# Optimization experiments

Hardware: AMD Instinct MI355X
Metric: run time of the kernel (lower is better)

## Reference

```python
import jax, jax.numpy as jnp
import numpy as np

NUM_HEADS = 12
STEP_SIZE = 3

def softmax_1(a):
    # exp(a_i) / (1 + sum_j exp(a_j)), numerically stable
    m = jnp.maximum(jnp.max(a, axis=-1, keepdims=True), 0.0)
    e = jnp.exp(a - m)
    return e / (jnp.exp(-m) + jnp.sum(e, axis=-1, keepdims=True))

def setup_inputs() -> dict:
    key = jax.random.key(0)
    ks = jax.random.split(key, 7)
    B, N, C, L = 16, 4096, 768, 16
    s = C ** -0.5
    return {
        "x": jax.random.normal(ks[0], (B, N, C), dtype=jnp.float32),
        "query": jax.random.normal(ks[1], (1, L, C), dtype=jnp.float32),
        "Wq": jax.random.normal(ks[2], (C, C), dtype=jnp.float32) * s,
        "Wk": jax.random.normal(ks[3], (C, C), dtype=jnp.float32) * s,
        "Wv": jax.random.normal(ks[4], (C, C), dtype=jnp.float32) * s,
        "Wproj": jax.random.normal(ks[5], (C, C), dtype=jnp.float32) * s,
        "b_proj": jnp.zeros((C,), dtype=jnp.float32),
    }

def reference(x, query, Wq, Wk, Wv, Wproj, b_proj):
    B, N, C = x.shape
    H = NUM_HEADS
    hd = C // H
    L = query.shape[1]
    scale = hd ** -0.5
    # learned queries broadcast over batch
    queries = jnp.broadcast_to(query, (B, L, C))
    q = (queries @ Wq.T).reshape(B, L, H, hd).transpose(0, 2, 1, 3)  # [B,H,L,hd]
    k = (x @ Wk.T).reshape(B, N, H, hd).transpose(0, 2, 1, 3)        # [B,H,N,hd]
    v = k  # Hopfield update: state retrieves against stored patterns k
    for _ in range(STEP_SIZE):
        qs = q * scale
        attn = jnp.einsum('bhld,bhnd->bhln', qs, k)  # [B,H,L,N]
        attn = softmax_1(attn)
        q = jnp.einsum('bhln,bhnd->bhld', attn, v)   # [B,H,L,hd]
    out = q.transpose(0, 2, 1, 3).reshape(B, L, C)
    out = out @ Wv.T          # self.v output projection (no bias)
    out = out @ Wproj.T + b_proj  # self.proj
    return out
```

## Files before the change

kernel.cpp:

```cpp
#include <hip/hip_runtime.h>


typedef float  float4v  __attribute__((ext_vector_type(4)));
typedef short  short4v  __attribute__((ext_vector_type(4)));
typedef short  short8v  __attribute__((ext_vector_type(8)));
typedef unsigned int uint4v __attribute__((ext_vector_type(4)));
typedef short8v bf16x8;

__device__ __forceinline__ void splitbf(float v, unsigned int& hi, unsigned int& lo){
  unsigned int u = __float_as_uint(v);
  hi = u >> 16;
  float r = v - __uint_as_float(u & 0xffff0000u);
  lo = (__float_as_uint(r) + 0x8000u) >> 16;
}
__device__ __forceinline__ unsigned int packbf(float v){
  unsigned int u = __float_as_uint(v);
  float r = v - __uint_as_float(u & 0xffff0000u);
  return (u >> 16) | ((__float_as_uint(r) + 0x8000u) & 0xffff0000u);
}

__global__ __launch_bounds__(256)
void cvt_planar_kernel(const float* __restrict__ src, unsigned short* __restrict__ dh,
                       unsigned short* __restrict__ dl){
  size_t idx = (size_t)blockIdx.x*256 + threadIdx.x;
  float4v v = ((const float4v*)src)[idx];
  short4v h4, l4;
  #pragma unroll
  for(int e=0;e<4;e++){
    unsigned int hh, ll;
    splitbf(v[e], hh, ll);
    h4[e] = (short)hh;
    l4[e] = (short)ll;
  }
  ((short4v*)dh)[idx] = h4;
  ((short4v*)dl)[idx] = l4;
}

__global__ __launch_bounds__(256)
void q0_kernel(const float* __restrict__ query, const float* __restrict__ wq,
               float* __restrict__ q0){
  int idx = blockIdx.x*256 + threadIdx.x;
  int l = idx / 768, c = idx - l*768;
  const float* qr = query + l*768;
  const float* wr = wq + (size_t)c*768;
  float s = 0.f;
  for(int j=0;j<768;j+=4){
    float4v a  = *(const float4v*)(qr+j);
    float4v w4 = *(const float4v*)(wr+j);
    s += a[0]*w4[0]+a[1]*w4[1]+a[2]*w4[2]+a[3]*w4[3];
  }
  q0[idx] = s;
}

__global__ __launch_bounds__(256, 3)
void gemm_k_kernel(const float* __restrict__ x, const unsigned short* __restrict__ wh,
                   const unsigned short* __restrict__ wl, unsigned int* __restrict__ khead){
  __shared__ unsigned short Ah[512*8], Al[512*8];
  const int tid  = threadIdx.x;
  const int id   = blockIdx.x;
  const int xcd  = id & 7, slot = id >> 3;
  const int bml  = slot / 6;
  const int bn   = slot - bml*6;
  const int bm   = xcd*64 + bml;
  const int wave = tid >> 6, lane = tid & 63, quad = lane >> 4, l16 = lane & 15;

  float4v acc[8][2];
  #pragma unroll
  for(int i=0;i<8;i++)
    #pragma unroll
    for(int j=0;j<2;j++) acc[i][j] = (float4v){0.f,0.f,0.f,0.f};

  const float* xA = x + (size_t)bm*128*768;
  const unsigned short* wbh = wh + (size_t)(bn*128 + wave*32 + l16)*768 + quad*8;
  const unsigned short* wbl = wl + (size_t)(bn*128 + wave*32 + l16)*768 + quad*8;

  const int row0 = tid >> 2, c8 = tid & 3;
  const int C0 = row0*4 + (c8 ^ ((row0 >> 2) & 3));
  const int C1 = C0 + 256;
  const float* g0 = xA + (size_t)row0*768 + c8*8;
  const float* g1 = g0 + (size_t)64*768;
  const int crd = l16*4 + (quad ^ ((l16 >> 2) & 3));

  float4v p00 = *(const float4v*)(g0);
  float4v p01 = *(const float4v*)(g0 + 4);
  float4v p10 = *(const float4v*)(g1);
  float4v p11 = *(const float4v*)(g1 + 4);

  for(int k0=0;k0<768;k0+=32){
    bf16x8 b_h[2], b_l[2];
    #pragma unroll
    for(int j=0;j<2;j++){
      b_h[j] = *(const bf16x8*)(wbh + (size_t)j*16*768 + k0);
      b_l[j] = *(const bf16x8*)(wbl + (size_t)j*16*768 + k0);
    }
    __syncthreads();

    {
      short8v hv, lv;
      #pragma unroll
      for(int e=0;e<4;e++){
        unsigned int hh, ll;
        splitbf(p00[e], hh, ll); hv[e]   = (short)hh; lv[e]   = (short)ll;
        splitbf(p01[e], hh, ll); hv[e+4] = (short)hh; lv[e+4] = (short)ll;
      }
      *(short8v*)(Ah + C0*8) = hv;
      *(short8v*)(Al + C0*8) = lv;
      #pragma unroll
      for(int e=0;e<4;e++){
        unsigned int hh, ll;
        splitbf(p10[e], hh, ll); hv[e]   = (short)hh; lv[e]   = (short)ll;
        splitbf(p11[e], hh, ll); hv[e+4] = (short)hh; lv[e+4] = (short)ll;
      }
      *(short8v*)(Ah + C1*8) = hv;
      *(short8v*)(Al + C1*8) = lv;
    }
    __syncthreads();

    if(k0 + 32 < 768){
      p00 = *(const float4v*)(g0 + k0 + 32);
      p01 = *(const float4v*)(g0 + k0 + 36);
      p10 = *(const float4v*)(g1 + k0 + 32);
      p11 = *(const float4v*)(g1 + k0 + 36);
    }

    #pragma unroll
    for(int i=0;i<8;i++){
      const unsigned short* ap = Ah + (size_t)(i*64 + crd)*8;
      const unsigned short* lp = Al + (size_t)(i*64 + crd)*8;
      bf16x8 a_h = *(const bf16x8*)ap;
      bf16x8 a_l = *(const bf16x8*)lp;
      #pragma unroll
      for(int j=0;j<2;j++){
        acc[i][j] = __builtin_amdgcn_mfma_f32_16x16x32_bf16(a_h, b_h[j], acc[i][j],0,0,0);
        acc[i][j] = __builtin_amdgcn_mfma_f32_16x16x32_bf16(a_l, b_h[j], acc[i][j],0,0,0);
        acc[i][j] = __builtin_amdgcn_mfma_f32_16x16x32_bf16(a_h, b_l[j], acc[i][j],0,0,0);
      }
    }
  }
  const int b     = bm >> 5;
  const int Cbase = bn*128 + wave*32;
  const int h     = Cbase >> 6;
  const int dbase = Cbase & 63;
  const int nn0   = (bm & 31)*128;
  unsigned int* kout = khead + ((size_t)(b*12 + h)*4096 + nn0)*64 + dbase;
  #pragma unroll
  for(int i=0;i<8;i++)
    #pragma unroll
    for(int j=0;j<2;j++)
      #pragma unroll
      for(int r=0;r<4;r++)
        kout[(size_t)(i*16 + quad*4 + r)*64 + j*16 + l16] = packbf(acc[i][j][r]);
}

__global__ __launch_bounds__(512, 2)
void attn3_kernel(const unsigned int* __restrict__ khead,
                  const float* __restrict__ q0g, float* __restrict__ qcur){
  __shared__ unsigned int knd[256*64];
  float* accf  = (float*)knd;
  float* lredf = (float*)knd + 8192;
  float* qtmp  = (float*)knd + 8320;

  const int tid  = threadIdx.x;
  const int bh   = blockIdx.x;
  const int b    = bh / 12;
  const int h    = bh - b*12;
  const int wave = tid >> 6, lane = tid & 63, quad = lane >> 4, l16 = lane & 15;

  const unsigned int* kb = khead + (size_t)(b*12 + h)*4096*64;
  const int srow = tid >> 1, scol = (tid & 1)*32;
  const int sphi = ((srow & 7) << 2) ^ ((srow & 8) << 1);
  const unsigned int* kbt = kb + (size_t)srow*64 + scol;

  const int rowA = wave*32 + ((l16 >> 2) << 3) + (l16 & 3);
  const int rowB = rowA + 4;
  const int phiA = ((l16 & 3) << 2) ^ (((l16 >> 2) & 1) << 4);
  const int phiB = phiA ^ 16;
  const int q1   = quad & 1;

  uint4v pf[8];
  #pragma unroll
  for(int g=0; g<8; ++g) pf[g] = *(const uint4v*)(kbt + g*4);

  for(int iter = 0; iter < 3; ++iter){
    const float* qrow = (iter == 0) ? (q0g + (size_t)l16*768 + h*64)
                                    : (qtmp + l16*64);
    bf16x8 qh[2], ql[2];
    #pragma unroll
    for(int s = 0; s < 2; ++s){
      float4v v0 = *(const float4v*)(qrow + s*32 + quad*8);
      float4v v1 = *(const float4v*)(qrow + s*32 + quad*8 + 4);
      #pragma unroll
      for(int e = 0; e < 8; ++e){
        float v = (e < 4 ? v0[e] : v1[e-4]) * 0.125f;
        unsigned int hh, ll;
        splitbf(v, hh, ll);
        qh[s][e] = (short)hh;
        ql[s][e] = (short)ll;
      }
    }
    __syncthreads();

    float4v acc[4];
    #pragma unroll
    for(int j=0;j<4;j++) acc[j] = (float4v){0.f,0.f,0.f,0.f};
    float lsum = 0.f;

    for(int t = 0; t < 16; ++t){
      #pragma unroll
      for(int g=0; g<8; ++g)
        *(uint4v*)(knd + srow*64 + ((scol + g*4) ^ sphi)) = pf[g];
      if(!(iter == 2 && t == 15)){
        const int tn = (t + 1) & 15;
        #pragma unroll
        for(int g=0; g<8; ++g) pf[g] = *(const uint4v*)(kbt + (size_t)tn*16384 + g*4);
      }

      float4v s1 = (float4v){0.f,0.f,0.f,0.f};
      float4v s2 = (float4v){0.f,0.f,0.f,0.f};
      #pragma unroll
      for(int s = 0; s < 2; ++s){
        const int c0 = s*32 + quad*8;
        uint4v w0 = *(const uint4v*)(knd + rowA*64 + ((c0    ) ^ phiA));
        uint4v w1 = *(const uint4v*)(knd + rowA*64 + ((c0 + 4) ^ phiA));
        uint4v u0 = *(const uint4v*)(knd + rowB*64 + ((c0    ) ^ phiB));
        uint4v u1 = *(const uint4v*)(knd + rowB*64 + ((c0 + 4) ^ phiB));
        bf16x8 a1h, a1l, a2h, a2l;
        #pragma unroll
        for(int j = 0; j < 4; ++j){
          a1h[j]   = (short)(w0[j] & 0xffffu);  a1l[j]   = (short)(w0[j] >> 16);
          a1h[j+4] = (short)(w1[j] & 0xffffu);  a1l[j+4] = (short)(w1[j] >> 16);
          a2h[j]   = (short)(u0[j] & 0xffffu);  a2l[j]   = (short)(u0[j] >> 16);
          a2h[j+4] = (short)(u1[j] & 0xffffu);  a2l[j+4] = (short)(u1[j] >> 16);
        }
        s1 = __builtin_amdgcn_mfma_f32_16x16x32_bf16(a1h, qh[s], s1, 0,0,0);
        s1 = __builtin_amdgcn_mfma_f32_16x16x32_bf16(a1l, qh[s], s1, 0,0,0);
        s1 = __builtin_amdgcn_mfma_f32_16x16x32_bf16(a1h, ql[s], s1, 0,0,0);
        s2 = __builtin_amdgcn_mfma_f32_16x16x32_bf16(a2h, qh[s], s2, 0,0,0);
        s2 = __builtin_amdgcn_mfma_f32_16x16x32_bf16(a2l, qh[s], s2, 0,0,0);
        s2 = __builtin_amdgcn_mfma_f32_16x16x32_bf16(a2h, ql[s], s2, 0,0,0);
      }

      bf16x8 pa_h, pa_l;
      #pragma unroll
      for(int e = 0; e < 4; ++e){
        float v = __expf(s1[e]);
        lsum += v;
        unsigned int hh, ll;
        splitbf(v, hh, ll);
        pa_h[e] = (short)hh;
        pa_l[e] = (short)ll;
        float v2 = __expf(s2[e]);
        lsum += v2;
        splitbf(v2, hh, ll);
        pa_h[e+4] = (short)hh;
        pa_l[e+4] = (short)ll;
      }

      const int rb0 = wave*32 + quad*8;
      #pragma unroll
      for(int j = 0; j < 4; ++j){
        bf16x8 kbh, kbl;
        #pragma unroll
        for(int e = 0; e < 8; ++e){
          const int jx = ((e >> 2) ^ q1) & 1;
          unsigned int w = knd[(rb0 + e)*64 + ((j ^ jx) << 4) + (l16 ^ ((e & 3) << 2))];
          kbh[e] = (short)(w & 0xffffu);
          kbl[e] = (short)(w >> 16);
        }
        acc[j] = __builtin_amdgcn_mfma_f32_16x16x32_bf16(pa_h, kbh, acc[j], 0,0,0);
        acc[j] = __builtin_amdgcn_mfma_f32_16x16x32_bf16(pa_l, kbh, acc[j], 0,0,0);
        acc[j] = __builtin_amdgcn_mfma_f32_16x16x32_bf16(pa_h, kbl, acc[j], 0,0,0);
      }
    }

    __syncthreads();
    lsum += __shfl_xor(lsum, 16);
    lsum += __shfl_xor(lsum, 32);
    if(quad == 0) lredf[wave*16 + l16] = lsum;
    #pragma unroll
    for(int j = 0; j < 4; ++j)
      #pragma unroll
      for(int r = 0; r < 4; ++r)
        accf[wave*1024 + (quad*4 + r)*64 + j*16 + l16] = acc[j][r];
    __syncthreads();
    #pragma unroll
    for(int k = 0; k < 2; ++k){
      const int i = tid + k*512;
      const int l = i >> 6, d = i & 63;
      float s = 0.f, lt = 1.f;
      #pragma unroll
      for(int w = 0; w < 8; ++w){ s += accf[w*1024 + i]; }
      #pragma unroll
      for(int w = 0; w < 8; ++w){ lt += lredf[w*16 + l]; }
      const float qv = s / lt;
      if(iter < 2) qtmp[i] = qv;
      else qcur[(size_t)(b*16 + l)*768 + h*64 + d] = qv;
    }
    __syncthreads();
  }
}

__global__ __launch_bounds__(256)
void proj_kernel(const float* __restrict__ inp, const float* __restrict__ w,
                 const float* __restrict__ bias, float* __restrict__ out){
  __shared__ float rows[4*768];
  const int r0 = blockIdx.x*4;
  const int c  = blockIdx.y*256 + threadIdx.x;
  for(int j = threadIdx.x; j < 4*768; j += 256) rows[j] = inp[(size_t)r0*768 + j];
  __syncthreads();
  const float* wr = w + (size_t)c*768;
  float a0=0.f, a1=0.f, a2=0.f, a3=0.f;
  for(int j=0;j<768;j+=4){
    float4v w4 = *(const float4v*)(wr+j);
    float4v r0v = *(const float4v*)(rows+j);
    float4v r1v = *(const float4v*)(rows+768+j);
    float4v r2v = *(const float4v*)(rows+1536+j);
    float4v r3v = *(const float4v*)(rows+2304+j);
    #pragma unroll
    for(int e=0;e<4;e++){
      a0 += r0v[e]*w4[e]; a1 += r1v[e]*w4[e];
      a2 += r2v[e]*w4[e]; a3 += r3v[e]*w4[e];
    }
  }
  const float bb = bias ? bias[c] : 0.f;
  out[(size_t)(r0+0)*768 + c] = a0 + bb;
  out[(size_t)(r0+1)*768 + c] = a1 + bb;
  out[(size_t)(r0+2)*768 + c] = a2 + bb;
  out[(size_t)(r0+3)*768 + c] = a3 + bb;
}

extern "C" void kernel_launch(void* const* d_in, const int* in_sizes, int n_in,
                              void* d_out, int out_size, void* d_ws, size_t ws_size,
                              hipStream_t stream){
  const float* x     = (const float*)d_in[0];
  const float* query = (const float*)d_in[1];
  const float* Wq    = (const float*)d_in[2];
  const float* Wk    = (const float*)d_in[3];
  const float* Wv    = (const float*)d_in[4];
  const float* Wproj = (const float*)d_in[5];
  const float* bproj = (const float*)d_in[6];
  float* out = (float*)d_out;

  char* ws = (char*)d_ws;
  unsigned int*   khead = (unsigned int*)(ws);
  float*          qcur  = (float*)(ws + 201326592);
  float*          q0    = (float*)(ws + 202113024);
  char*           R     = ws + 202162176;
  unsigned short* wkh   = (unsigned short*)(R);
  unsigned short* wkl   = (unsigned short*)(R + 1179648);
  float*          out1  = (float*)(R);

  cvt_planar_kernel<<<576, 256, 0, stream>>>(Wk, wkh, wkl);
  q0_kernel<<<48, 256, 0, stream>>>(query, Wq, q0);
  gemm_k_kernel<<<3072, 256, 0, stream>>>(x, wkh, wkl, khead);

  attn3_kernel<<<192, 512, 0, stream>>>(khead, q0, qcur);

  proj_kernel<<<dim3(64, 3), 256, 0, stream>>>(qcur, Wv, nullptr, out1);
  proj_kernel<<<dim3(64, 3), 256, 0, stream>>>(out1, Wproj, bproj, out);
}
```

Baseline: 682.6 us.

## Double-buffer LDS tiles in K-projection GEMM with one barrier per step

The K-projection GEMM now ping-pongs between two LDS buffers. Each step converts and stores the next x tile into one buffer while running MFMAs on the other, so there is one barrier per k-step instead of two. Global loads for x and the weight fragments are issued two and one steps ahead. This raises LDS use to 32KB per block and adds register pressure, which could lower occupancy under the 3-blocks-per-CU launch bound.

Result: slower. 784.8 us (+15.0%).

```diff
diff --git a/kernel.cpp b/kernel.cpp
--- a/kernel.cpp
+++ b/kernel.cpp
@@ -52,10 +52,52 @@
   q0[idx] = s;
 }
 
+__device__ __forceinline__ void conv_store(unsigned short* __restrict__ AhW,
+                                           unsigned short* __restrict__ AlW,
+                                           int C0, int C1,
+                                           float4v p0, float4v p1, float4v p2, float4v p3){
+  short8v hv, lv;
+  #pragma unroll
+  for(int e=0;e<4;e++){
+    unsigned int hh, ll;
+    splitbf(p0[e], hh, ll); hv[e]   = (short)hh; lv[e]   = (short)ll;
+    splitbf(p1[e], hh, ll); hv[e+4] = (short)hh; lv[e+4] = (short)ll;
+  }
+  *(short8v*)(AhW + C0*8) = hv;
+  *(short8v*)(AlW + C0*8) = lv;
+  #pragma unroll
+  for(int e=0;e<4;e++){
+    unsigned int hh, ll;
+    splitbf(p2[e], hh, ll); hv[e]   = (short)hh; lv[e]   = (short)ll;
+    splitbf(p3[e], hh, ll); hv[e+4] = (short)hh; lv[e+4] = (short)ll;
+  }
+  *(short8v*)(AhW + C1*8) = hv;
+  *(short8v*)(AlW + C1*8) = lv;
+}
+
+__device__ __forceinline__ void mfma_phase(const unsigned short* __restrict__ AhR,
+                                           const unsigned short* __restrict__ AlR,
+                                           int crd,
+                                           bf16x8 bh0, bf16x8 bh1, bf16x8 bl0, bf16x8 bl1,
+                                           float4v (&acc)[8][2]){
+  #pragma unroll
+  for(int i=0;i<8;i++){
+    bf16x8 a_h = *(const bf16x8*)(AhR + (size_t)(i*64 + crd)*8);
+    bf16x8 a_l = *(const bf16x8*)(AlR + (size_t)(i*64 + crd)*8);
+    acc[i][0] = __builtin_amdgcn_mfma_f32_16x16x32_bf16(a_h, bh0, acc[i][0],0,0,0);
+    acc[i][0] = __builtin_amdgcn_mfma_f32_16x16x32_bf16(a_l, bh0, acc[i][0],0,0,0);
+    acc[i][0] = __builtin_amdgcn_mfma_f32_16x16x32_bf16(a_h, bl0, acc[i][0],0,0,0);
+    acc[i][1] = __builtin_amdgcn_mfma_f32_16x16x32_bf16(a_h, bh1, acc[i][1],0,0,0);
+    acc[i][1] = __builtin_amdgcn_mfma_f32_16x16x32_bf16(a_l, bh1, acc[i][1],0,0,0);
+    acc[i][1] = __builtin_amdgcn_mfma_f32_16x16x32_bf16(a_h, bl1, acc[i][1],0,0,0);
+  }
+}
+
 __global__ __launch_bounds__(256, 3)
 void gemm_k_kernel(const float* __restrict__ x, const unsigned short* __restrict__ wh,
                    const unsigned short* __restrict__ wl, unsigned int* __restrict__ khead){
-  __shared__ unsigned short Ah[512*8], Al[512*8];
+  __shared__ unsigned short Ah0[512*8], Al0[512*8];
+  __shared__ unsigned short Ah1[512*8], Al1[512*8];
   const int tid  = threadIdx.x;
   const int id   = blockIdx.x;
   const int xcd  = id & 7, slot = id >> 3;
@@ -81,62 +123,42 @@
   const float* g1 = g0 + (size_t)64*768;
   const int crd = l16*4 + (quad ^ ((l16 >> 2) & 3));
 
-  float4v p00 = *(const float4v*)(g0);
-  float4v p01 = *(const float4v*)(g0 + 4);
-  float4v p10 = *(const float4v*)(g1);
-  float4v p11 = *(const float4v*)(g1 + 4);
-
-  for(int k0=0;k0<768;k0+=32){
-    bf16x8 b_h[2], b_l[2];
-    #pragma unroll
-    for(int j=0;j<2;j++){
-      b_h[j] = *(const bf16x8*)(wbh + (size_t)j*16*768 + k0);
-      b_l[j] = *(const bf16x8*)(wbl + (size_t)j*16*768 + k0);
-    }
-    __syncthreads();
-
+  float4v pA0, pA1, pA2, pA3, pB0, pB1, pB2, pB3;
+  bf16x8 bCh0, bCh1, bCl0, bCl1, bNh0, bNh1, bNl0, bNl1;
+  pA0 = *(const float4v*)(g0);      pA1 = *(const float4v*)(g0 + 4);
+  pA2 = *(const float4v*)(g1);      pA3 = *(const float4v*)(g1 + 4);
+  pB0 = *(const float4v*)(g0 + 32); pB1 = *(const float4v*)(g0 + 36);
+  pB2 = *(const float4v*)(g1 + 32); pB3 = *(const float4v*)(g1 + 36);
+  bCh0 = *(const bf16x8*)(wbh);          bCh1 = *(const bf16x8*)(wbh + 12288);
+  bCl0 = *(const bf16x8*)(wbl);          bCl1 = *(const bf16x8*)(wbl + 12288);
+  conv_store(Ah0, Al0, C0, C1, pA0, pA1, pA2, pA3);
+  __syncthreads();
+
+  for(int i = 0; i < 12; ++i){
     {
-      short8v hv, lv;
-      #pragma unroll
-      for(int e=0;e<4;e++){
-        unsigned int hh, ll;
-        splitbf(p00[e], hh, ll); hv[e]   = (short)hh; lv[e]   = (short)ll;
-        splitbf(p01[e], hh, ll); hv[e+4] = (short)hh; lv[e+4] = (short)ll;
-      }
-      *(short8v*)(Ah + C0*8) = hv;
-      *(short8v*)(Al + C0*8) = lv;
-      #pragma unroll
-      for(int e=0;e<4;e++){
-        unsigned int hh, ll;
-        splitbf(p10[e], hh, ll); hv[e]   = (short)hh; lv[e]   = (short)ll;
-        splitbf(p11[e], hh, ll); hv[e+4] = (short)hh; lv[e+4] = (short)ll;
-      }
-      *(short8v*)(Ah + C1*8) = hv;
-      *(short8v*)(Al + C1*8) = lv;
-    }
-    __syncthreads();
-
-    if(k0 + 32 < 768){
-      p00 = *(const float4v*)(g0 + k0 + 32);
-      p01 = *(const float4v*)(g0 + k0 + 36);
-      p10 = *(const float4v*)(g1 + k0 + 32);
-      p11 = *(const float4v*)(g1 + k0 + 36);
-    }
-
-    #pragma unroll
-    for(int i=0;i<8;i++){
-      const unsigned short* ap = Ah + (size_t)(i*64 + crd)*8;
-      const unsigned short* lp = Al + (size_t)(i*64 + crd)*8;
-      bf16x8 a_h = *(const bf16x8*)ap;
-      bf16x8 a_l = *(const bf16x8*)lp;
-      #pragma unroll
-      for(int j=0;j<2;j++){
-        acc[i][j] = __builtin_amdgcn_mfma_f32_16x16x32_bf16(a_h, b_h[j], acc[i][j],0,0,0);
-        acc[i][j] = __builtin_amdgcn_mfma_f32_16x16x32_bf16(a_l, b_h[j], acc[i][j],0,0,0);
-        acc[i][j] = __builtin_amdgcn_mfma_f32_16x16x32_bf16(a_h, b_l[j], acc[i][j],0,0,0);
-      }
-    }
-  }
+      const int ka = (2*i + 2 < 24) ? (2*i + 2)*32 : 736;
+      const int kb = (2*i + 1)*32;
+      pA0 = *(const float4v*)(g0 + ka); pA1 = *(const float4v*)(g0 + ka + 4);
+      pA2 = *(const float4v*)(g1 + ka); pA3 = *(const float4v*)(g1 + ka + 4);
+      bNh0 = *(const bf16x8*)(wbh + kb); bNh1 = *(const bf16x8*)(wbh + 12288 + kb);
+      bNl0 = *(const bf16x8*)(wbl + kb); bNl1 = *(const bf16x8*)(wbl + 12288 + kb);
+      conv_store(Ah1, Al1, C0, C1, pB0, pB1, pB2, pB3);
+      mfma_phase(Ah0, Al0, crd, bCh0, bCh1, bCl0, bCl1, acc);
+      __syncthreads();
+    }
+    {
+      const int ka = (2*i + 3 < 24) ? (2*i + 3)*32 : 736;
+      const int kb = (2*i + 2 < 24) ? (2*i + 2)*32 : 736;
+      pB0 = *(const float4v*)(g0 + ka); pB1 = *(const float4v*)(g0 + ka + 4);
+      pB2 = *(const float4v*)(g1 + ka); pB3 = *(const float4v*)(g1 + ka + 4);
+      bCh0 = *(const bf16x8*)(wbh + kb); bCh1 = *(const bf16x8*)(wbh + 12288 + kb);
+      bCl0 = *(const bf16x8*)(wbl + kb); bCl1 = *(const bf16x8*)(wbl + 12288 + kb);
+      conv_store(Ah0, Al0, C0, C1, pA0, pA1, pA2, pA3);
+      mfma_phase(Ah1, Al1, crd, bNh0, bNh1, bNl0, bNl1, acc);
+      __syncthreads();
+    }
+  }
+
   const int b     = bm >> 5;
   const int Cbase = bn*128 + wave*32;
   const int h     = Cbase >> 6;
```

## Split Hopfield attention over N into four chunks with atomic cross-block reduction

Applied to the files above, without the earlier changes.

The single attention kernel that ran all three Hopfield iterations in one block per (batch, head) is split into a per-iteration partial kernel. It launches four blocks per (batch, head), each covering a quarter of the keys, and accumulates partial outputs and softmax denominators with global atomics. A small reduce kernel then normalizes and resets the accumulators. This raises the grid from 192 to 768 blocks to fill the GPU's compute units. The cost is extra kernel launches, atomic traffic and nondeterministic float summation order.

After: 810.1 us. 18.7% more time.

```diff
diff --git a/kernel.cpp b/kernel.cpp
--- a/kernel.cpp
+++ b/kernel.cpp
@@ -52,6 +52,11 @@
   q0[idx] = s;
 }
 
+__global__ __launch_bounds__(512)
+void zero_kernel(float* __restrict__ p){
+  p[(size_t)blockIdx.x*512 + threadIdx.x] = 0.f;
+}
+
 __global__ __launch_bounds__(256, 3)
 void gemm_k_kernel(const float* __restrict__ x, const unsigned short* __restrict__ wh,
                    const unsigned short* __restrict__ wl, unsigned int* __restrict__ khead){
@@ -152,21 +157,23 @@
         kout[(size_t)(i*16 + quad*4 + r)*64 + j*16 + l16] = packbf(acc[i][j][r]);
 }
 
-__global__ __launch_bounds__(512, 2)
-void attn3_kernel(const unsigned int* __restrict__ khead,
-                  const float* __restrict__ q0g, float* __restrict__ qcur){
+__global__ __launch_bounds__(512, 4)
+void attn_part_kernel(const unsigned int* __restrict__ khead,
+                      const float* __restrict__ q0g,
+                      const float* __restrict__ qred,
+                      int first,
+                      float* __restrict__ gacc, float* __restrict__ glsum){
   __shared__ unsigned int knd[256*64];
   float* accf  = (float*)knd;
   float* lredf = (float*)knd + 8192;
-  float* qtmp  = (float*)knd + 8320;
-
-  const int tid  = threadIdx.x;
-  const int bh   = blockIdx.x;
-  const int b    = bh / 12;
-  const int h    = bh - b*12;
-  const int wave = tid >> 6, lane = tid & 63, quad = lane >> 4, l16 = lane & 15;
-
-  const unsigned int* kb = khead + (size_t)(b*12 + h)*4096*64;
+
+  const int tid   = threadIdx.x;
+  const int bh    = blockIdx.x >> 2;
+  const int chunk = blockIdx.x & 3;
+  const int h     = bh - (bh/12)*12;
+  const int wave  = tid >> 6, lane = tid & 63, quad = lane >> 4, l16 = lane & 15;
+
+  const unsigned int* kb = khead + (size_t)bh*4096*64 + (size_t)chunk*4*16384;
   const int srow = tid >> 1, scol = (tid & 1)*32;
   const int sphi = ((srow & 7) << 2) ^ ((srow & 8) << 1);
   const unsigned int* kbt = kb + (size_t)srow*64 + scol;
@@ -177,127 +184,143 @@
   const int phiB = phiA ^ 16;
   const int q1   = quad & 1;
 
+  const float* qrow = first ? (q0g + (size_t)l16*768 + h*64)
+                            : (qred + (size_t)bh*1024 + l16*64);
+  bf16x8 qh[2], ql[2];
+  #pragma unroll
+  for(int s = 0; s < 2; ++s){
+    float4v v0 = *(const float4v*)(qrow + s*32 + quad*8);
+    float4v v1 = *(const float4v*)(qrow + s*32 + quad*8 + 4);
+    #pragma unroll
+    for(int e = 0; e < 8; ++e){
+      float v = (e < 4 ? v0[e] : v1[e-4]) * 0.125f;
+      unsigned int hh, ll;
+      splitbf(v, hh, ll);
+      qh[s][e] = (short)hh;
+      ql[s][e] = (short)ll;
+    }
+  }
+
   uint4v pf[8];
   #pragma unroll
   for(int g=0; g<8; ++g) pf[g] = *(const uint4v*)(kbt + g*4);
 
-  for(int iter = 0; iter < 3; ++iter){
-    const float* qrow = (iter == 0) ? (q0g + (size_t)l16*768 + h*64)
-                                    : (qtmp + l16*64);
-    bf16x8 qh[2], ql[2];
+  float4v acc[4];
+  #pragma unroll
+  for(int j=0;j<4;j++) acc[j] = (float4v){0.f,0.f,0.f,0.f};
+  float lsum = 0.f;
+
+  for(int t = 0; t < 4; ++t){
+    #pragma unroll
+    for(int g=0; g<8; ++g)
+      *(uint4v*)(knd + srow*64 + ((scol + g*4) ^ sphi)) = pf[g];
+    if(t < 3){
+      #pragma unroll
+      for(int g=0; g<8; ++g) pf[g] = *(const uint4v*)(kbt + (size_t)(t+1)*16384 + g*4);
+    }
+
+    float4v s1 = (float4v){0.f,0.f,0.f,0.f};
+    float4v s2 = (float4v){0.f,0.f,0.f,0.f};
     #pragma unroll
     for(int s = 0; s < 2; ++s){
-      float4v v0 = *(const float4v*)(qrow + s*32 + quad*8);
-      float4v v1 = *(const float4v*)(qrow + s*32 + quad*8 + 4);
+      const int c0 = s*32 + quad*8;
+      uint4v w0 = *(const uint4v*)(knd + rowA*64 + ((c0    ) ^ phiA));
+      uint4v w1 = *(const uint4v*)(knd + rowA*64 + ((c0 + 4) ^ phiA));
+      uint4v u0 = *(const uint4v*)(knd + rowB*64 + ((c0    ) ^ phiB));
+      uint4v u1 = *(const uint4v*)(knd + rowB*64 + ((c0 + 4) ^ phiB));
+      bf16x8 a1h, a1l, a2h, a2l;
+      #pragma unroll
+      for(int j = 0; j < 4; ++j){
+        a1h[j]   = (short)(w0[j] & 0xffffu);  a1l[j]   = (short)(w0[j] >> 16);
+        a1h[j+4] = (short)(w1[j] & 0xffffu);  a1l[j+4] = (short)(w1[j] >> 16);
+        a2h[j]   = (short)(u0[j] & 0xffffu);  a2l[j]   = (short)(u0[j] >> 16);
+        a2h[j+4] = (short)(u1[j] & 0xffffu);  a2l[j+4] = (short)(u1[j] >> 16);
+      }
+      s1 = __builtin_amdgcn_mfma_f32_16x16x32_bf16(a1h, qh[s], s1, 0,0,0);
+      s1 = __builtin_amdgcn_mfma_f32_16x16x32_bf16(a1l, qh[s], s1, 0,0,0);
+      s1 = __builtin_amdgcn_mfma_f32_16x16x32_bf16(a1h, ql[s], s1, 0,0,0);
+      s2 = __builtin_amdgcn_mfma_f32_16x16x32_bf16(a2h, qh[s], s2, 0,0,0);
+      s2 = __builtin_amdgcn_mfma_f32_16x16x32_bf16(a2l, qh[s], s2, 0,0,0);
+      s2 = __builtin_amdgcn_mfma_f32_16x16x32_bf16(a2h, ql[s], s2, 0,0,0);
+    }
+
+    bf16x8 pa_h, pa_l;
+    #pragma unroll
+    for(int e = 0; e < 4; ++e){
+      float v = __expf(s1[e]);
+      lsum += v;
+      unsigned int hh, ll;
+      splitbf(v, hh, ll);
+      pa_h[e] = (short)hh;
+      pa_l[e] = (short)ll;
+      float v2 = __expf(s2[e]);
+      lsum += v2;
+      splitbf(v2, hh, ll);
+      pa_h[e+4] = (short)hh;
+      pa_l[e+4] = (short)ll;
+    }
+
+    const int rb0 = wave*32 + quad*8;
+    #pragma unroll
+    for(int j = 0; j < 4; ++j){
+      bf16x8 kbh, kbl;
       #pragma unroll
       for(int e = 0; e < 8; ++e){
-        float v = (e < 4 ? v0[e] : v1[e-4]) * 0.125f;
-        unsigned int hh, ll;
-        splitbf(v, hh, ll);
-        qh[s][e] = (short)hh;
-        ql[s][e] = (short)ll;
-      }
-    }
-    __syncthreads();
-
-    float4v acc[4];
-    #pragma unroll
-    for(int j=0;j<4;j++) acc[j] = (float4v){0.f,0.f,0.f,0.f};
-    float lsum = 0.f;
-
-    for(int t = 0; t < 16; ++t){
-      #pragma unroll
-      for(int g=0; g<8; ++g)
-        *(uint4v*)(knd + srow*64 + ((scol + g*4) ^ sphi)) = pf[g];
-      if(!(iter == 2 && t == 15)){
-        const int tn = (t + 1) & 15;
-        #pragma unroll
-        for(int g=0; g<8; ++g) pf[g] = *(const uint4v*)(kbt + (size_t)tn*16384 + g*4);
-      }
-
-      float4v s1 = (float4v){0.f,0.f,0.f,0.f};
-      float4v s2 = (float4v){0.f,0.f,0.f,0.f};
-      #pragma unroll
-      for(int s = 0; s < 2; ++s){
-        const int c0 = s*32 + quad*8;
-        uint4v w0 = *(const uint4v*)(knd + rowA*64 + ((c0    ) ^ phiA));
-        uint4v w1 = *(const uint4v*)(knd + rowA*64 + ((c0 + 4) ^ phiA));
-        uint4v u0 = *(const uint4v*)(knd + rowB*64 + ((c0    ) ^ phiB));
-        uint4v u1 = *(const uint4v*)(knd + rowB*64 + ((c0 + 4) ^ phiB));
-        bf16x8 a1h, a1l, a2h, a2l;
-        #pragma unroll
-        for(int j = 0; j < 4; ++j){
-          a1h[j]   = (short)(w0[j] & 0xffffu);  a1l[j]   = (short)(w0[j] >> 16);
-          a1h[j+4] = (short)(w1[j] & 0xffffu);  a1l[j+4] = (short)(w1[j] >> 16);
-          a2h[j]   = (short)(u0[j] & 0xffffu);  a2l[j]   = (short)(u0[j] >> 16);
-          a2h[j+4] = (short)(u1[j] & 0xffffu);  a2l[j+4] = (short)(u1[j] >> 16);
-        }
-        s1 = __builtin_amdgcn_mfma_f32_16x16x32_bf16(a1h, qh[s], s1, 0,0,0);
-        s1 = __builtin_amdgcn_mfma_f32_16x16x32_bf16(a1l, qh[s], s1, 0,0,0);
-        s1 = __builtin_amdgcn_mfma_f32_16x16x32_bf16(a1h, ql[s], s1, 0,0,0);
-        s2 = __builtin_amdgcn_mfma_f32_16x16x32_bf16(a2h, qh[s], s2, 0,0,0);
-        s2 = __builtin_amdgcn_mfma_f32_16x16x32_bf16(a2l, qh[s], s2, 0,0,0);
-        s2 = __builtin_amdgcn_mfma_f32_16x16x32_bf16(a2h, ql[s], s2, 0,0,0);
-      }
-
-      bf16x8 pa_h, pa_l;
-      #pragma unroll
-      for(int e = 0; e < 4; ++e){
-        float v = __expf(s1[e]);
-        lsum += v;
-        unsigned int hh, ll;
-        splitbf(v, hh, ll);
-        pa_h[e] = (short)hh;
-        pa_l[e] = (short)ll;
-        float v2 = __expf(s2[e]);
-        lsum += v2;
-        splitbf(v2, hh, ll);
-        pa_h[e+4] = (short)hh;
-        pa_l[e+4] = (short)ll;
-      }
-
-      const int rb0 = wave*32 + quad*8;
-      #pragma unroll
-      for(int j = 0; j < 4; ++j){
-        bf16x8 kbh, kbl;
-        #pragma unroll
-        for(int e = 0; e < 8; ++e){
-          const int jx = ((e >> 2) ^ q1) & 1;
-          unsigned int w = knd[(rb0 + e)*64 + ((j ^ jx) << 4) + (l16 ^ ((e & 3) << 2))];
-          kbh[e] = (short)(w & 0xffffu);
-          kbl[e] = (short)(w >> 16);
-        }
-        acc[j] = __builtin_amdgcn_mfma_f32_16x16x32_bf16(pa_h, kbh, acc[j], 0,0,0);
-        acc[j] = __builtin_amdgcn_mfma_f32_16x16x32_bf16(pa_l, kbh, acc[j], 0,0,0);
-        acc[j] = __builtin_amdgcn_mfma_f32_16x16x32_bf16(pa_h, kbl, acc[j], 0,0,0);
-      }
-    }
-
-    __syncthreads();
-    lsum += __shfl_xor(lsum, 16);
-    lsum += __shfl_xor(lsum, 32);
-    if(quad == 0) lredf[wave*16 + l16] = lsum;
-    #pragma unroll
-    for(int j = 0; j < 4; ++j)
-      #pragma unroll
-      for(int r = 0; r < 4; ++r)
-        accf[wave*1024 + (quad*4 + r)*64 + j*16 + l16] = acc[j][r];
-    __syncthreads();
-    #pragma unroll
-    for(int k = 0; k < 2; ++k){
-      const int i = tid + k*512;
-      const int l = i >> 6, d = i & 63;
-      float s = 0.f, lt = 1.f;
-      #pragma unroll
-      for(int w = 0; w < 8; ++w){ s += accf[w*1024 + i]; }
-      #pragma unroll
-      for(int w = 0; w < 8; ++w){ lt += lredf[w*16 + l]; }
-      const float qv = s / lt;
-      if(iter < 2) qtmp[i] = qv;
-      else qcur[(size_t)(b*16 + l)*768 + h*64 + d] = qv;
-    }
-    __syncthreads();
-  }
+        const int jx = ((e >> 2) ^ q1) & 1;
+        unsigned int w = knd[(rb0 + e)*64 + ((j ^ jx) << 4) + (l16 ^ ((e & 3) << 2))];
+        kbh[e] = (short)(w & 0xffffu);
+        kbl[e] = (short)(w >> 16);
+      }
+      acc[j] = __builtin_amdgcn_mfma_f32_16x16x32_bf16(pa_h, kbh, acc[j], 0,0,0);
+      acc[j] = __builtin_amdgcn_mfma_f32_16x16x32_bf16(pa_l, kbh, acc[j], 0,0,0);
+      acc[j] = __builtin_amdgcn_mfma_f32_16x16x32_bf16(pa_h, kbl, acc[j], 0,0,0);
+    }
+  }
+
+  __syncthreads();
+  lsum += __shfl_xor(lsum, 16);
+  lsum += __shfl_xor(lsum, 32);
+  if(quad == 0) lredf[wave*16 + l16] = lsum;
+  #pragma unroll
+  for(int j = 0; j < 4; ++j)
+    #pragma unroll
+    for(int r = 0; r < 4; ++r)
+      accf[wave*1024 + (quad*4 + r)*64 + j*16 + l16] = acc[j][r];
+  __syncthreads();
+  #pragma unroll
+  for(int k = 0; k < 2; ++k){
+    const int i = tid + k*512;
+    float s = 0.f;
+    #pragma unroll
+    for(int w = 0; w < 8; ++w){ s += accf[w*1024 + i]; }
+    atomicAdd(&gacc[(size_t)bh*1024 + i], s);
+  }
+  if(tid < 16){
+    float lt = 0.f;
+    #pragma unroll
+    for(int w = 0; w < 8; ++w){ lt += lredf[w*16 + tid]; }
+    atomicAdd(&glsum[bh*16 + tid], lt);
+  }
+}
+
+__global__ __launch_bounds__(256)
+void attn_reduce_kernel(float* __restrict__ gacc, float* __restrict__ glsum,
+                        float* __restrict__ qred, float* __restrict__ qcur,
+                        int final){
+  const int bh = blockIdx.x;
+  const int b  = bh / 12, h = bh - b*12;
+  #pragma unroll
+  for(int k = 0; k < 4; ++k){
+    const int i = threadIdx.x + k*256;
+    const int l = i >> 6, d = i & 63;
+    const float s  = gacc[(size_t)bh*1024 + i];
+    const float lt = 1.f + glsum[bh*16 + l];
+    const float qv = s / lt;
+    if(final) qcur[(size_t)(b*16 + l)*768 + h*64 + d] = qv;
+    else      qred[(size_t)bh*1024 + i] = qv;
+    gacc[(size_t)bh*1024 + i] = 0.f;
+  }
+  if(threadIdx.x < 16) glsum[bh*16 + threadIdx.x] = 0.f;
 }
 
 __global__ __launch_bounds__(256)
@@ -348,13 +371,23 @@
   char*           R     = ws + 202162176;
   unsigned short* wkh   = (unsigned short*)(R);
   unsigned short* wkl   = (unsigned short*)(R + 1179648);
+  float*          gacc  = (float*)(R);
+  float*          glsum = (float*)(R + 786432);
+  float*          qred  = (float*)(R + 798720);
   float*          out1  = (float*)(R);
 
   cvt_planar_kernel<<<576, 256, 0, stream>>>(Wk, wkh, wkl);
   q0_kernel<<<48, 256, 0, stream>>>(query, Wq, q0);
   gemm_k_kernel<<<3072, 256, 0, stream>>>(x, wkh, wkl, khead);
 
-  attn3_kernel<<<192, 512, 0, stream>>>(khead, q0, qcur);
+  zero_kernel<<<390, 512, 0, stream>>>(gacc);
+
+  for(int it = 0; it < 3; ++it){
+    attn_part_kernel<<<768, 512, 0, stream>>>(khead, q0, qred, it == 0 ? 1 : 0,
+                                              gacc, glsum);
+    attn_reduce_kernel<<<192, 256, 0, stream>>>(gacc, glsum, qred, qcur,
+                                                it == 2 ? 1 : 0);
+  }
 
   proj_kernel<<<dim3(64, 3), 256, 0, stream>>>(qcur, Wv, nullptr, out1);
   proj_kernel<<<dim3(64, 3), 256, 0, stream>>>(out1, Wproj, bproj, out);
```

## Load K tiles straight into double-buffered LDS with pre-swizzled layout

Applied to the files above, without the earlier changes.

The K-projection kernel now writes K in an LDS-ready tiled layout, with the XOR swizzle already applied per 256-row tile. The attention kernel then uses global_load_lds to DMA each tile directly into one of two LDS buffers, waiting only on vmcnt. This removes the register staging of prefetched K and the separate LDS store pass, and overlaps the next tile's load with compute on the current one. In exchange, the K buffer doubles to 128KB of LDS, which likely cuts the two-blocks-per-CU occupancy requested by the launch bounds down to one. It also relies on each wave reading only the rows it loaded itself, since there is no block barrier between tiles.

Result: faster. 663.6 us (-2.8%).

```diff
diff --git a/kernel.cpp b/kernel.cpp
--- a/kernel.cpp
+++ b/kernel.cpp
@@ -17,6 +17,12 @@
   unsigned int u = __float_as_uint(v);
   float r = v - __uint_as_float(u & 0xffff0000u);
   return (u >> 16) | ((__float_as_uint(r) + 0x8000u) & 0xffff0000u);
+}
+
+__device__ __forceinline__ void gll16(const unsigned int* g, unsigned int* l){
+  __builtin_amdgcn_global_load_lds(
+      (const __attribute__((address_space(1))) unsigned int*)g,
+      (__attribute__((address_space(3))) unsigned int*)l, 16, 0, 0);
 }
 
 __global__ __launch_bounds__(256)
@@ -142,23 +148,29 @@
   const int h     = Cbase >> 6;
   const int dbase = Cbase & 63;
   const int nn0   = (bm & 31)*128;
-  unsigned int* kout = khead + ((size_t)(b*12 + h)*4096 + nn0)*64 + dbase;
+  unsigned int* kout = khead + (size_t)(b*12 + h)*262144;
   #pragma unroll
-  for(int i=0;i<8;i++)
-    #pragma unroll
-    for(int j=0;j<2;j++)
-      #pragma unroll
-      for(int r=0;r<4;r++)
-        kout[(size_t)(i*16 + quad*4 + r)*64 + j*16 + l16] = packbf(acc[i][j][r]);
+  for(int i=0;i<8;i++){
+    #pragma unroll
+    for(int r=0;r<4;r++){
+      const int n   = nn0 + i*16 + quad*4 + r;
+      const int row = n & 255, t = n >> 8;
+      const int ph  = ((row & 7) << 2) ^ ((row & 8) << 1);
+      unsigned int* kr = kout + (size_t)t*16384 + row*64;
+      #pragma unroll
+      for(int j=0;j<2;j++)
+        kr[(dbase + j*16 + l16) ^ ph] = packbf(acc[i][j][r]);
+    }
+  }
 }
 
 __global__ __launch_bounds__(512, 2)
 void attn3_kernel(const unsigned int* __restrict__ khead,
                   const float* __restrict__ q0g, float* __restrict__ qcur){
-  __shared__ unsigned int knd[256*64];
-  float* accf  = (float*)knd;
-  float* lredf = (float*)knd + 8192;
-  float* qtmp  = (float*)knd + 8320;
+  __shared__ unsigned int knd[2*16384];
+  float* accf  = (float*)(knd + 16384);
+  float* lredf = (float*)(knd + 16384) + 8192;
+  float* qtmp  = (float*)(knd + 16384) + 8320;
 
   const int tid  = threadIdx.x;
   const int bh   = blockIdx.x;
@@ -166,10 +178,9 @@
   const int h    = bh - b*12;
   const int wave = tid >> 6, lane = tid & 63, quad = lane >> 4, l16 = lane & 15;
 
-  const unsigned int* kb = khead + (size_t)(b*12 + h)*4096*64;
-  const int srow = tid >> 1, scol = (tid & 1)*32;
-  const int sphi = ((srow & 7) << 2) ^ ((srow & 8) << 1);
-  const unsigned int* kbt = kb + (size_t)srow*64 + scol;
+  const unsigned int* kg = khead + (size_t)bh*262144;
+  const unsigned int* kwv = kg + wave*2048 + lane*4;
+  unsigned int* lwv = knd + wave*2048;
 
   const int rowA = wave*32 + ((l16 >> 2) << 3) + (l16 & 3);
   const int rowB = rowA + 4;
@@ -177,9 +188,8 @@
   const int phiB = phiA ^ 16;
   const int q1   = quad & 1;
 
-  uint4v pf[8];
   #pragma unroll
-  for(int g=0; g<8; ++g) pf[g] = *(const uint4v*)(kbt + g*4);
+  for(int g=0; g<8; ++g) gll16(kwv + g*256, lwv + g*256);
 
   for(int iter = 0; iter < 3; ++iter){
     const float* qrow = (iter == 0) ? (q0g + (size_t)l16*768 + h*64)
@@ -206,13 +216,17 @@
     float lsum = 0.f;
 
     for(int t = 0; t < 16; ++t){
-      #pragma unroll
-      for(int g=0; g<8; ++g)
-        *(uint4v*)(knd + srow*64 + ((scol + g*4) ^ sphi)) = pf[g];
+      const unsigned int* kcur = knd + ((t & 1) << 14);
+
+      asm volatile("s_waitcnt vmcnt(0)" ::: "memory");
+      __builtin_amdgcn_sched_barrier(0);
+
       if(!(iter == 2 && t == 15)){
         const int tn = (t + 1) & 15;
+        const unsigned int* gsrc = kwv + (size_t)tn*16384;
+        unsigned int* ldst = lwv + (((t + 1) & 1) << 14);
         #pragma unroll
-        for(int g=0; g<8; ++g) pf[g] = *(const uint4v*)(kbt + (size_t)tn*16384 + g*4);
+        for(int g=0; g<8; ++g) gll16(gsrc + g*256, ldst + g*256);
       }
 
       float4v s1 = (float4v){0.f,0.f,0.f,0.f};
@@ -220,10 +234,10 @@
       #pragma unroll
       for(int s = 0; s < 2; ++s){
         const int c0 = s*32 + quad*8;
-        uint4v w0 = *(const uint4v*)(knd + rowA*64 + ((c0    ) ^ phiA));
-        uint4v w1 = *(const uint4v*)(knd + rowA*64 + ((c0 + 4) ^ phiA));
-        uint4v u0 = *(const uint4v*)(knd + rowB*64 + ((c0    ) ^ phiB));
-        uint4v u1 = *(const uint4v*)(knd + rowB*64 + ((c0 + 4) ^ phiB));
+        uint4v w0 = *(const uint4v*)(kcur + rowA*64 + ((c0    ) ^ phiA));
+        uint4v w1 = *(const uint4v*)(kcur + rowA*64 + ((c0 + 4) ^ phiA));
+        uint4v u0 = *(const uint4v*)(kcur + rowB*64 + ((c0    ) ^ phiB));
+        uint4v u1 = *(const uint4v*)(kcur + rowB*64 + ((c0 + 4) ^ phiB));
         bf16x8 a1h, a1l, a2h, a2l;
         #pragma unroll
         for(int j = 0; j < 4; ++j){
@@ -263,7 +277,7 @@
         #pragma unroll
         for(int e = 0; e < 8; ++e){
           const int jx = ((e >> 2) ^ q1) & 1;
-          unsigned int w = knd[(rb0 + e)*64 + ((j ^ jx) << 4) + (l16 ^ ((e & 3) << 2))];
+          unsigned int w = kcur[(rb0 + e)*64 + ((j ^ jx) << 4) + (l16 ^ ((e & 3) << 2))];
           kbh[e] = (short)(w & 0xffffu);
           kbl[e] = (short)(w >> 16);
         }
```
